# Optimization experiments

Measured on AMD Instinct MI355X. Metric: run time of the kernel, lower is better.

## Reference

```python
import jax, jax.numpy as jnp
import numpy as np

N, C, H, W = 64, 256, 28, 28
INTER = 128  # in_channels // reduction
STD = 0.01   # init std of the 1x1 convs


def setup_inputs() -> dict:
    key = jax.random.key(0)
    k_x, k_idx, k_wq, k_wv, k_lam = jax.random.split(key, 5)
    x = jax.random.normal(k_x, (N, C, H, W), dtype=jnp.float32)
    lam = jax.random.uniform(k_lam, (), dtype=jnp.float32)
    index = jax.random.randint(k_idx, (N,), 0, N)
    # query 1x1 conv (shared for q and k since x_qk_concat=False -> key is None)
    Wq = jax.random.normal(k_wq, (INTER, C), dtype=jnp.float32) * STD
    bq = jnp.zeros((INTER,), dtype=jnp.float32)
    # value 1x1 conv -> 1 channel
    Wv = jax.random.normal(k_wv, (1, C), dtype=jnp.float32) * STD
    bv = jnp.zeros((1,), dtype=jnp.float32)
    return {"x": x, "lam": lam, "index": index, "Wq": Wq, "bq": bq,
            "Wv": Wv, "bv": bv, "scale_factor": 8}


def _conv1x1(x, w, b):
    # x: [n,c,h,w], w: [o,c], b: [o] -> [n,o,h,w]
    return jnp.einsum('nchw,oc->nohw', x, w) + b[None, :, None, None]


def reference(x, lam, index, Wq, bq, Wv, bv, scale_factor):
    n, c, h, w = x.shape
    hw = h * w
    x_lam = x               # [n,c,h,w]
    x_lam_ = x[index]       # shuffled pair
    # value: 1x1 conv to 1 channel -> [n, hw, 1]
    v = _conv1x1(x_lam_, Wv, bv).reshape(n, 1, hw).transpose(0, 2, 1)
    # query / key share the same conv (key is None when x_qk_concat=False)
    q = _conv1x1(x_lam, Wq, bq).reshape(n, INTER, hw).transpose(0, 2, 1)  # [n,hw,inter]
    k = _conv1x1(x_lam_, Wq, bq).reshape(n, INTER, hw)                    # [n,inter,hw]
    # embedded gaussian similarity, forced fp32, scaled by sqrt(inter)
    scores = jnp.einsum('nqc,nck->nqk', q.astype(jnp.float32), k.astype(jnp.float32))
    scores = scores / jnp.float32(np.sqrt(INTER))
    pw = jax.nn.softmax(scores, axis=-1)  # [n,hw,hw]
    mask = jnp.einsum('nqk,nko->nqo', pw, v.astype(jnp.float32)).reshape(n, 1, h, w)
    # bilinear upsample (align_corners=False semantics) then sigmoid
    mask = jax.image.resize(mask, (n, 1, h * scale_factor, w * scale_factor),
                            method='bilinear')
    mask = jax.nn.sigmoid(mask)
    # results['mask'] = cat([1 - m, m], dim=1)
    return jnp.concatenate([1.0 - mask, mask], axis=1)
```

## Files before the change

### kernel.cpp

```cpp
#include <hip/hip_runtime.h>
#include <math.h>

#define NB    64
#define CIN   256
#define HH    28
#define WW    28
#define HW    784
#define INTER 128

typedef __bf16 bf16x8 __attribute__((ext_vector_type(8)));
typedef float  f32x4  __attribute__((ext_vector_type(4)));

#define SCALE 0.35709723f

#define GLB(p) ((const __attribute__((address_space(1))) void*)(p))
#define LDSP(p) ((__attribute__((address_space(3))) void*)(p))


__device__ __forceinline__ unsigned int bfbits(float f) {
    unsigned int u = __builtin_bit_cast(unsigned int, f);
    return (u + 0x7fffu + ((u >> 16) & 1u)) >> 16;
}

__global__ __launch_bounds__(256) void initw_kernel(
    const float* __restrict__ Wq, unsigned short* __restrict__ Wbh)
{
    const int e  = blockIdx.x * 256 + threadIdx.x;
    const int j  = e & 7;
    const int l  = (e >> 3) & 63;
    const int it = (e >> 9) & 7;
    const int s  = e >> 12;
    const int i  = it * 16 + (l & 15);
    const int c  = s * 32 + ((l >> 4) & 3) * 8 + j;
    Wbh[e] = (unsigned short)bfbits(Wq[i * CIN + c] * SCALE);
}

__global__ __launch_bounds__(256, 5) void proj_kernel(
    const float* __restrict__ x,
    const unsigned short* __restrict__ Wfh,
    const float* __restrict__ bq,
    const float* __restrict__ Wv, const float* __restrict__ bv,
    unsigned short* __restrict__ Yb, float* __restrict__ vAll)
{
    __shared__ float          Xs [2][32 * 64];
    __shared__ unsigned short Whs[2][4096];

    const int ptile = blockIdx.x;
    const int n     = blockIdx.y;
    const int t     = threadIdx.x;
    const int l     = t & 63;
    const int w     = t >> 6;
    const int pl    = l & 15;
    const int g     = l >> 4;
    const int p0    = ptile * 64;

    const float* xn = x + (size_t)n * (CIN * HW);

    const int kk    = pl ^ (w << 2);
    const int psrc  = min(p0 + kk * 4, HW - 4);

    const int slot  = ((w * 16 + pl) >> 2) ^ (g << 2);
    const int rbyte = slot * 4 + (pl & 3);

    f32x4 acc[8];
#pragma unroll
    for (int it = 0; it < 8; ++it) acc[it] = (f32x4){0.f, 0.f, 0.f, 0.f};
    float vpart = 0.0f;

#pragma unroll
    for (int q = 0; q < 2; ++q) {
        const int rt = w * 8 + q * 4 + g;
        __builtin_amdgcn_global_load_lds(GLB(xn + (size_t)rt * HW + psrc),
                                         LDSP(&Xs[0][(w * 8 + q * 4) * 64]), 16, 0, 0);
        const int chunk = (w * 2 + q) * 512;
        __builtin_amdgcn_global_load_lds(GLB(Wfh + chunk + l * 8),
                                         LDSP(&Whs[0][chunk]), 16, 0, 0);
    }
    __syncthreads();

    int cur = 0;
    for (int s = 0; s < 8; ++s) {
        if (s < 7) {
#pragma unroll
            for (int q = 0; q < 2; ++q) {
                const int rt = w * 8 + q * 4 + g;
                __builtin_amdgcn_global_load_lds(
                    GLB(xn + (size_t)((s + 1) * 32 + rt) * HW + psrc),
                    LDSP(&Xs[cur ^ 1][(w * 8 + q * 4) * 64]), 16, 0, 0);
                const int chunk = (w * 2 + q) * 512;
                __builtin_amdgcn_global_load_lds(
                    GLB(Wfh + (s + 1) * 4096 + chunk + l * 8),
                    LDSP(&Whs[cur ^ 1][chunk]), 16, 0, 0);
            }
        }

        float xv[8];
#pragma unroll
        for (int j = 0; j < 8; ++j)
            xv[j] = Xs[cur][(g * 8 + j) * 64 + rbyte];

        const float4 wv0 = *(const float4*)(Wv + s * 32 + g * 8);
        const float4 wv1 = *(const float4*)(Wv + s * 32 + g * 8 + 4);
        vpart = fmaf(xv[0], wv0.x, fmaf(xv[1], wv0.y,
                fmaf(xv[2], wv0.z, fmaf(xv[3], wv0.w, vpart))));
        vpart = fmaf(xv[4], wv1.x, fmaf(xv[5], wv1.y,
                fmaf(xv[6], wv1.z, fmaf(xv[7], wv1.w, vpart))));

        bf16x8 ah;
#pragma unroll
        for (int j = 0; j < 8; ++j) ah[j] = (__bf16)xv[j];

#pragma unroll
        for (int it = 0; it < 8; ++it) {
            const bf16x8 wh = *(const bf16x8*)&Whs[cur][it * 512 + l * 8];
            acc[it] = __builtin_amdgcn_mfma_f32_16x16x32_bf16(ah, wh, acc[it], 0, 0, 0);
        }

        __syncthreads();
        cur ^= 1;
    }

    const int p0w = p0 + w * 16;

    vpart += __shfl_xor(vpart, 16);
    vpart += __shfl_xor(vpart, 32);
    if (g == 0 && p0w + pl < HW)
        vAll[n * HW + p0w + pl] = vpart + bv[0];

#pragma unroll
    for (int it = 0; it < 8; ++it) {
        const int i = it * 16 + pl;
        const float bb = bq[i] * SCALE;
#pragma unroll
        for (int r = 0; r < 4; ++r) {
            const int pr = p0w + g * 4 + r;
            if (pr < HW)
                Yb[((size_t)n * HW + pr) * INTER + i] =
                    (unsigned short)bfbits(acc[it][r] + bb);
        }
    }
}

__global__ __launch_bounds__(256) void attn_kernel(
    const unsigned short* __restrict__ Yb, const float* __restrict__ vAll,
    const int* __restrict__ index, float* __restrict__ maskbuf)
{
    __shared__ float red[2][4][112];

    const int n   = blockIdx.x;
    const int qt  = blockIdx.y;
    const int q0  = qt * 112;
    const int t   = threadIdx.x;
    const int l   = t & 63;
    const int w   = t >> 6;
    const int idx = index[n];

    const unsigned short* Qg = Yb + (size_t)n   * (HW * INTER);
    const unsigned short* Kg = Yb + (size_t)idx * (HW * INTER);
    const float*          Vg = vAll + (size_t)idx * HW;

    const int ql = l & 15;
    const int g  = l >> 4;

    bf16x8 qf[7][4];
#pragma unroll
    for (int qg = 0; qg < 7; ++qg) {
        const int qrow = q0 + qg * 16 + ql;
#pragma unroll
        for (int ic = 0; ic < 4; ++ic)
            qf[qg][ic] = *(const bf16x8*)(Qg + (size_t)qrow * INTER + ic * 32 + g * 8);
    }

    float ll[7] = {0.f, 0.f, 0.f, 0.f, 0.f, 0.f, 0.f};
    float oo[7] = {0.f, 0.f, 0.f, 0.f, 0.f, 0.f, 0.f};

    const int NT = (w == 0) ? 13 : 12;
    const unsigned short* Ka = Kg + (size_t)(w * 16 + ql) * INTER + g * 8;
    const float*          Va = Vg + w * 16 + g * 4;

    bf16x8 afA[4], afB[4];
    float4 vvA, vvB;

#define LOADK(kt, dst, vdst)                                               \
    {                                                                      \
        const unsigned short* kp = Ka + (size_t)(kt) * (64 * INTER);       \
        dst[0] = *(const bf16x8*)(kp);                                     \
        dst[1] = *(const bf16x8*)(kp + 32);                                \
        dst[2] = *(const bf16x8*)(kp + 64);                                \
        dst[3] = *(const bf16x8*)(kp + 96);                                \
        vdst = *(const float4*)(Va + (kt) * 64);                           \
    }

#define PROCESS(af, vv)                                                    \
    {                                                                      \
        _Pragma("unroll")                                                  \
        for (int qg = 0; qg < 7; ++qg) {                                   \
            f32x4 acc = (f32x4){0.f, 0.f, 0.f, 0.f};                       \
            _Pragma("unroll")                                              \
            for (int ic = 0; ic < 4; ++ic)                                 \
                acc = __builtin_amdgcn_mfma_f32_16x16x32_bf16(             \
                    af[ic], qf[qg][ic], acc, 0, 0, 0);                     \
            const float e0 = exp2f(acc[0]);                                \
            const float e1 = exp2f(acc[1]);                                \
            const float e2 = exp2f(acc[2]);                                \
            const float e3 = exp2f(acc[3]);                                \
            ll[qg] += (e0 + e1) + (e2 + e3);                               \
            oo[qg] = fmaf(e0, vv.x, fmaf(e1, vv.y,                         \
                     fmaf(e2, vv.z, fmaf(e3, vv.w, oo[qg]))));             \
        }                                                                  \
    }

    LOADK(0, afA, vvA);
    int kt = 0;
    for (; kt + 1 < NT; kt += 2) {
        LOADK(kt + 1, afB, vvB);
        PROCESS(afA, vvA);
        if (kt + 2 < NT) LOADK(kt + 2, afA, vvA);
        PROCESS(afB, vvB);
    }
    if (kt < NT) PROCESS(afA, vvA);

#undef LOADK
#undef PROCESS

#pragma unroll
    for (int qg = 0; qg < 7; ++qg) {
        ll[qg] += __shfl_xor(ll[qg], 16); ll[qg] += __shfl_xor(ll[qg], 32);
        oo[qg] += __shfl_xor(oo[qg], 16); oo[qg] += __shfl_xor(oo[qg], 32);
    }
    if (g == 0) {
#pragma unroll
        for (int qg = 0; qg < 7; ++qg) {
            red[0][w][qg * 16 + ql] = ll[qg];
            red[1][w][qg * 16 + ql] = oo[qg];
        }
    }
    __syncthreads();
    if (t < 112) {
        const float L = red[0][0][t] + red[0][1][t] + red[0][2][t] + red[0][3][t];
        const float O = red[1][0][t] + red[1][1][t] + red[1][2][t] + red[1][3][t];
        maskbuf[n * HW + q0 + t] = O / L;
    }
}

__global__ __launch_bounds__(256) void upsample_kernel(
    const float* __restrict__ maskbuf, float* __restrict__ out)
{
    const int gid = blockIdx.x * 256 + threadIdx.x;
    const int n  = gid / (224 * 56);
    const int r  = gid - n * (224 * 56);
    const int oy = r / 56;
    const int xq = r - oy * 56;

    const float iy = (oy + 0.5f) * 0.125f - 0.5f;
    const int   y0 = (int)floorf(iy);
    const float fy = iy - (float)y0;
    const int y0c = max(y0, 0), y1c = min(y0 + 1, HH - 1);
    const float* mrow = maskbuf + n * HW;

    float res[4];
#pragma unroll
    for (int j = 0; j < 4; ++j) {
        const int   ox = (xq << 2) + j;
        const float ix = (ox + 0.5f) * 0.125f - 0.5f;
        const int   x0 = (int)floorf(ix);
        const float fx = ix - (float)x0;
        const int x0c = max(x0, 0), x1c = min(x0 + 1, WW - 1);
        const float v00 = mrow[y0c * WW + x0c], v01 = mrow[y0c * WW + x1c];
        const float v10 = mrow[y1c * WW + x0c], v11 = mrow[y1c * WW + x1c];
        const float m = (v00 * (1.0f - fx) + v01 * fx) * (1.0f - fy)
                      + (v10 * (1.0f - fx) + v11 * fx) * fy;
        res[j] = 1.0f / (1.0f + __expf(-m));
    }

    float4 pos = make_float4(res[0], res[1], res[2], res[3]);
    float4 neg = make_float4(1.0f - res[0], 1.0f - res[1],
                             1.0f - res[2], 1.0f - res[3]);
    const size_t base = (size_t)n * 2 * 50176 + (size_t)oy * 224 + (xq << 2);
    *(float4*)(out + base)         = neg;
    *(float4*)(out + base + 50176) = pos;
}

extern "C" void kernel_launch(void* const* d_in, const int* in_sizes, int n_in,
                              void* d_out, int out_size, void* d_ws, size_t ws_size,
                              hipStream_t stream) {
    const float* x     = (const float*)d_in[0];
    const int*   index = (const int*)d_in[2];
    const float* Wq    = (const float*)d_in[3];
    const float* bq    = (const float*)d_in[4];
    const float* Wv    = (const float*)d_in[5];
    const float* bv    = (const float*)d_in[6];

    float* out = (float*)d_out;
    unsigned short* Yb  = (unsigned short*)d_out;
    unsigned short* Wbh = Yb + (size_t)NB * HW * INTER;
    float* vAll  = (float*)d_ws;
    float* maskb = vAll + NB * HW;

    initw_kernel<<<128, 256, 0, stream>>>(Wq, Wbh);
    proj_kernel<<<dim3(13, NB), 256, 0, stream>>>(x, Wbh, bq, Wv, bv, Yb, vAll);
    attn_kernel<<<dim3(NB, 7), 256, 0, stream>>>(Yb, vAll, index, maskb);
    upsample_kernel<<<3136, 256, 0, stream>>>(maskb, out);
}
```

Before: 62.19 us.

## Triple-buffer projection kernel loads with prefetch depth two and vmcnt waits

The projection kernel moves from a double-buffered LDS pipeline to a triple-buffered one. Tiles are issued two stages ahead, and each stage waits with a partial vmcnt followed by a single barrier, replacing the trailing __syncthreads. This is meant to hide more global-load latency and remove one barrier per iteration. In exchange, LDS use goes up and the launch-bounds occupancy hint drops from 5 to 3, so fewer blocks may be resident per CU. The only work in this kernel is the projection part of the whole pipeline.

```diff
diff --git a/kernel.cpp b/kernel.cpp
--- a/kernel.cpp
+++ b/kernel.cpp
@@ -15,7 +15,6 @@
 
 #define GLB(p) ((const __attribute__((address_space(1))) void*)(p))
 #define LDSP(p) ((__attribute__((address_space(3))) void*)(p))
-
 
 __device__ __forceinline__ unsigned int bfbits(float f) {
     unsigned int u = __builtin_bit_cast(unsigned int, f);
@@ -35,15 +34,15 @@
     Wbh[e] = (unsigned short)bfbits(Wq[i * CIN + c] * SCALE);
 }
 
-__global__ __launch_bounds__(256, 5) void proj_kernel(
+__global__ __launch_bounds__(256, 3) void proj_kernel(
     const float* __restrict__ x,
     const unsigned short* __restrict__ Wfh,
     const float* __restrict__ bq,
     const float* __restrict__ Wv, const float* __restrict__ bv,
     unsigned short* __restrict__ Yb, float* __restrict__ vAll)
 {
-    __shared__ float          Xs [2][32 * 64];
-    __shared__ unsigned short Whs[2][4096];
+    __shared__ float          Xs [3][32 * 64];
+    __shared__ unsigned short Whs[3][4096];
 
     const int ptile = blockIdx.x;
     const int n     = blockIdx.y;
@@ -67,32 +66,34 @@
     for (int it = 0; it < 8; ++it) acc[it] = (f32x4){0.f, 0.f, 0.f, 0.f};
     float vpart = 0.0f;
 
-#pragma unroll
-    for (int q = 0; q < 2; ++q) {
-        const int rt = w * 8 + q * 4 + g;
-        __builtin_amdgcn_global_load_lds(GLB(xn + (size_t)rt * HW + psrc),
-                                         LDSP(&Xs[0][(w * 8 + q * 4) * 64]), 16, 0, 0);
-        const int chunk = (w * 2 + q) * 512;
-        __builtin_amdgcn_global_load_lds(GLB(Wfh + chunk + l * 8),
-                                         LDSP(&Whs[0][chunk]), 16, 0, 0);
-    }
-    __syncthreads();
-
-    int cur = 0;
+#define PISSUE(tile_, buf_)                                                  \
+    {                                                                        \
+        _Pragma("unroll")                                                    \
+        for (int q = 0; q < 2; ++q) {                                        \
+            const int rt = w * 8 + q * 4 + g;                                \
+            __builtin_amdgcn_global_load_lds(                                \
+                GLB(xn + (size_t)((tile_) * 32 + rt) * HW + psrc),           \
+                LDSP(&Xs[buf_][(w * 8 + q * 4) * 64]), 16, 0, 0);            \
+            const int chunk = (w * 2 + q) * 512;                             \
+            __builtin_amdgcn_global_load_lds(                                \
+                GLB(Wfh + (tile_) * 4096 + chunk + l * 8),                   \
+                LDSP(&Whs[buf_][chunk]), 16, 0, 0);                          \
+        }                                                                    \
+    }
+
+    PISSUE(0, 0)
+    PISSUE(1, 1)
+
     for (int s = 0; s < 8; ++s) {
-        if (s < 7) {
-#pragma unroll
-            for (int q = 0; q < 2; ++q) {
-                const int rt = w * 8 + q * 4 + g;
-                __builtin_amdgcn_global_load_lds(
-                    GLB(xn + (size_t)((s + 1) * 32 + rt) * HW + psrc),
-                    LDSP(&Xs[cur ^ 1][(w * 8 + q * 4) * 64]), 16, 0, 0);
-                const int chunk = (w * 2 + q) * 512;
-                __builtin_amdgcn_global_load_lds(
-                    GLB(Wfh + (s + 1) * 4096 + chunk + l * 8),
-                    LDSP(&Whs[cur ^ 1][chunk]), 16, 0, 0);
-            }
-        }
+        if (s < 7) asm volatile("s_waitcnt vmcnt(4)" ::: "memory");
+        else       asm volatile("s_waitcnt vmcnt(0)" ::: "memory");
+        __builtin_amdgcn_sched_barrier(0);
+        __builtin_amdgcn_s_barrier();
+        __builtin_amdgcn_sched_barrier(0);
+
+        if (s + 2 < 8) PISSUE(s + 2, (s + 2) % 3)
+
+        const int cur = s % 3;
 
         float xv[8];
 #pragma unroll
@@ -115,10 +116,8 @@
             const bf16x8 wh = *(const bf16x8*)&Whs[cur][it * 512 + l * 8];
             acc[it] = __builtin_amdgcn_mfma_f32_16x16x32_bf16(ah, wh, acc[it], 0, 0, 0);
         }
-
-        __syncthreads();
-        cur ^= 1;
-    }
+    }
+#undef PISSUE
 
     const int p0w = p0 + w * 16;
 
```

Measured after the change: 69.77 us. +12.2%, slower.
